# Kernel tuning notes

Measured on AMD Instinct MI355X. Metric: run time of the kernel, lower is better.

Reference implementation:

```python
import jax, jax.numpy as jnp
import numpy as np

N = 100000   # real nodes
E = 100000   # real edges (tree-like rumor cascades)
B = 128      # graphs in batch
IN = 256     # in_feats
HID = 128    # GCN hidden
OUT = 128    # out_feats


def setup_inputs() -> dict:
    key = jax.random.key(0)
    ks = jax.random.split(key, 16)
    sc = lambda k, sh: (jax.random.normal(k, sh, jnp.float32) * 0.05)
    x = jax.random.normal(ks[0], (N, IN), jnp.float32)
    edge_index = jax.random.randint(ks[1], (2, E), 0, N, jnp.int32)
    # sorted segment ids, every graph non-empty (equal split)
    batch = ((jnp.arange(N, dtype=jnp.int32) * B) // N).astype(jnp.int32)
    return {
        "x": x,
        "emb_w": sc(ks[2], (1, IN)),
        "td_w1": sc(ks[3], (IN, HID)), "td_b1": sc(ks[4], (HID,)),
        "td_w2": sc(ks[5], (HID, OUT)), "td_b2": sc(ks[6], (OUT,)),
        "bu_w1": sc(ks[7], (IN, HID)), "bu_b1": sc(ks[8], (HID,)),
        "bu_w2": sc(ks[9], (HID, OUT)), "bu_b2": sc(ks[10], (OUT,)),
        "p_w1": sc(ks[11], (2 * OUT, 256)), "p_b1": sc(ks[12], (256,)),
        "p_w2": sc(ks[13], (256, 128)), "p_b2": sc(ks[14], (128,)),
        "edge_index": edge_index,
        "batch": batch,
        "num_graphs": B,
    }


def gcn_conv(h, src, dst, W, b, n):
    # PyG GCNConv: transform, add self-loops, symmetric normalization, scatter-add
    h = h @ W
    loops = jnp.arange(n, dtype=src.dtype)
    s = jnp.concatenate([src, loops])
    d = jnp.concatenate([dst, loops])
    deg = jax.ops.segment_sum(jnp.ones(s.shape, h.dtype), d, num_segments=n)
    dinv = jax.lax.rsqrt(deg)  # deg >= 1 thanks to self-loops
    norm = dinv[s] * dinv[d]
    out = jax.ops.segment_sum(h[s] * norm[:, None], d, num_segments=n)
    return out + b


def reference(x, emb_w, td_w1, td_b1, td_w2, td_b2,
              bu_w1, bu_b1, bu_w2, bu_b2,
              p_w1, p_b1, p_w2, p_b2,
              edge_index, batch, num_graphs):
    n = x.shape[0]
    nv = n + 1  # with virtual node
    xv = jnp.concatenate([x, emb_w], axis=0)
    # root = first node of each graph (batch is sorted)
    roots = jnp.searchsorted(batch, jnp.arange(num_graphs, dtype=batch.dtype)).astype(edge_index.dtype)
    vsrc = jnp.full((num_graphs,), n, edge_index.dtype)
    src = jnp.concatenate([edge_index[0], vsrc])
    dst = jnp.concatenate([edge_index[1], roots])

    def branch(s, d, w1, b1, w2, b2):
        h = jax.nn.relu(gcn_conv(xv, s, d, w1, b1, nv))
        # dropout is identity in eval mode
        h = gcn_conv(h, s, d, w2, b2, nv)
        # Prompt=True: pool real nodes, add virtual-node embedding
        return jax.ops.segment_sum(h[:-1], batch, num_segments=num_graphs) + h[-1]

    td = branch(src, dst, td_w1, td_b1, td_w2, td_b2)
    bu = branch(dst, src, bu_w1, bu_b1, bu_w2, bu_b2)  # flipped edges
    h = jnp.concatenate([bu, td], axis=1)  # [B, 2*OUT]
    return jax.nn.relu(h @ p_w1 + p_b1) @ p_w2 + p_b2  # [B, 128]
```

## Files before the change

kernel.cpp:

```cpp
#include <hip/hip_runtime.h>

typedef __bf16 bf16_t;
typedef __bf16 bf16x8 __attribute__((ext_vector_type(8)));
typedef float f32x4 __attribute__((ext_vector_type(4)));

#define INF 256
#define HF 128
#define NPB 16
#define CHP 16
#define SLMASK 0x00FFFFFF
#define SCAN_STRIDE 512

__device__ inline float2 bf2_to_f2(unsigned v) {
    float lo = __uint_as_float(v << 16);
    float hi = __uint_as_float(v & 0xffff0000u);
    return make_float2(lo, hi);
}
__device__ inline unsigned f2_to_bf2(float a, float b) {
    __bf16 x = (__bf16)a, y = (__bf16)b;
    unsigned short ux = __builtin_bit_cast(unsigned short, x);
    unsigned short uy = __builtin_bit_cast(unsigned short, y);
    return (unsigned)ux | ((unsigned)uy << 16);
}

__global__ void k_init(const int* __restrict__ batch, int* __restrict__ roots,
                       int* __restrict__ Z, int N, int B, int zwords) {
    int i = blockIdx.x * blockDim.x + threadIdx.x;
    if (i < zwords) Z[i] = 0;
    if (i == 0) roots[B] = N;
    if (i < N) {
        if (i == 0) roots[batch[0]] = 0;
        else if (batch[i] != batch[i - 1]) roots[batch[i]] = i;
    }
}

__global__ void k_wswz2(const float* __restrict__ tw1, const float* __restrict__ bw1,
                        bf16_t* __restrict__ o) {
    int idx = blockIdx.x * blockDim.x + threadIdx.x;
    if (idx >= 65536) return;
    const float* W = (idx < 32768) ? tw1 : bw1;
    bf16_t* out = o + (idx & 32768);
    int i = idx & 32767;
    int j  = i & 7;
    int l  = (i >> 3) & 63;
    int t  = i >> 9;
    int n  = t & 7;
    int kk = t >> 3;
    int k  = kk * 32 + ((l >> 4) << 3) + j;
    int c  = (n << 4) + (l & 15);
    out[i] = (bf16_t)W[k * HF + c];
}

__global__ void k_degboth(const int* __restrict__ src, const int* __restrict__ dst,
                          const int* __restrict__ roots, int* __restrict__ indeg,
                          int E, int B, int N, int nv) {
    int e = blockIdx.x * blockDim.x + threadIdx.x;
    if (e >= E + B) return;
    int a, b;
    if (e < E) { a = src[e]; b = dst[e]; }
    else       { a = N;      b = roots[e - E]; }
    atomicAdd(&indeg[b], 1);
    atomicAdd(&indeg[nv + a], 1);
}

__global__ void k_dinvboth(const int* __restrict__ indeg, float* __restrict__ dinv, int n2) {
    int i = blockIdx.x * blockDim.x + threadIdx.x;
    if (i < n2) dinv[i] = rsqrtf(1.0f + (float)indeg[i]);
}

__global__ __launch_bounds__(256) void k_scan1(const int* __restrict__ indeg, int* __restrict__ bsum, int nv) {
    int dir = blockIdx.y;
    __shared__ int s[256];
    int t = threadIdx.x;
    int v = blockIdx.x * 256 + t;
    s[t] = (v < nv) ? indeg[dir * nv + v] : 0;
    __syncthreads();
    for (int off = 128; off > 0; off >>= 1) {
        if (t < off) s[t] += s[t + off];
        __syncthreads();
    }
    if (t == 0) bsum[dir * SCAN_STRIDE + blockIdx.x] = s[0];
}

__global__ __launch_bounds__(512) void k_scan2(int* __restrict__ bsum, int nblk) {
    int dir = blockIdx.y;
    int* p = bsum + dir * SCAN_STRIDE;
    __shared__ int s[512];
    int t = threadIdx.x;
    int v = (t < nblk) ? p[t] : 0;
    s[t] = v;
    __syncthreads();
    for (int off = 1; off < 512; off <<= 1) {
        int u = (t >= off) ? s[t - off] : 0;
        __syncthreads();
        s[t] += u;
        __syncthreads();
    }
    if (t < nblk) p[t] = s[t] - v;
}

__global__ __launch_bounds__(256) void k_scan3(const int* __restrict__ indeg, const int* __restrict__ bsum,
                                               int* __restrict__ off, int* __restrict__ cursor,
                                               int nv, int total) {
    int dir = blockIdx.y;
    __shared__ int s[256];
    int t = threadIdx.x;
    int v0 = blockIdx.x * 256 + t;
    int val = (v0 < nv) ? indeg[dir * nv + v0] : 0;
    s[t] = val;
    __syncthreads();
    for (int o = 1; o < 256; o <<= 1) {
        int u = (t >= o) ? s[t - o] : 0;
        __syncthreads();
        s[t] += u;
        __syncthreads();
    }
    int excl = s[t] - val + bsum[dir * SCAN_STRIDE + blockIdx.x];
    if (v0 < nv) {
        off[dir * (nv + 1) + v0] = excl;
        cursor[dir * nv + v0] = excl;
    }
    if (blockIdx.x == 0 && t == 0) off[dir * (nv + 1) + nv] = total;
}

__global__ void k_fill(const int* __restrict__ src, const int* __restrict__ dst,
                       const int* __restrict__ roots, int* __restrict__ cursor,
                       int* __restrict__ slots,
                       int E, int B, int N, int nv) {
    int e = blockIdx.x * blockDim.x + threadIdx.x;
    if (e >= E + B) return;
    int EB = E + B;
    int a, b;
    if (e < E) { a = src[e]; b = dst[e]; }
    else       { a = N;      b = roots[e - E]; }
    int p = atomicAdd(&cursor[b], 1);
    slots[p] = a | ((b & (NPB - 1)) << 24);
    p = atomicAdd(&cursor[nv + a], 1);
    slots[EB + p] = b | ((a & (NPB - 1)) << 24);
}

__global__ __launch_bounds__(512) void k_gemm1both(
    const float* __restrict__ x, const float* __restrict__ emb,
    const bf16_t* __restrict__ WfTD, const bf16_t* __restrict__ WfBU,
    const float* __restrict__ dinvTD, const float* __restrict__ dinvBU,
    bf16_t* __restrict__ rawsTD, bf16_t* __restrict__ rawsBU,
    int nv, int N)
{
    __shared__ bf16_t WS[8192];
    int lane = threadIdx.x & 63;
    int wave = threadIdx.x >> 6;
    int rowbase = blockIdx.x * 128 + wave * 16;
    int r = rowbase + (lane & 15);
    int kseg = lane >> 4;
    const float* xr = (r < N) ? (x + (size_t)r * INF) : emb;

    auto stage = [&](int kk) {
        #pragma unroll
        for (int q = 0; q < 2; ++q) {
            int idx = q * 512 + threadIdx.x;
            int d = idx >> 9, r9 = idx & 511;
            const bf16_t* Wsrc = d ? WfBU : WfTD;
            *reinterpret_cast<float4*>(WS + (size_t)idx * 8) =
                *reinterpret_cast<const float4*>(Wsrc + ((size_t)(kk << 9) + r9) * 8);
        }
    };

    bf16x8 a[8];
    #pragma unroll
    for (int h = 0; h < 2; ++h) {
        float4 f[8];
        #pragma unroll
        for (int kk = 0; kk < 4; ++kk) {
            int k0 = (h * 4 + kk) * 32 + kseg * 8;
            f[2 * kk]     = *reinterpret_cast<const float4*>(xr + k0);
            f[2 * kk + 1] = *reinterpret_cast<const float4*>(xr + k0 + 4);
        }
        #pragma unroll
        for (int kk = 0; kk < 4; ++kk) {
            bf16x8 av;
            av[0] = (__bf16)f[2 * kk].x;     av[1] = (__bf16)f[2 * kk].y;
            av[2] = (__bf16)f[2 * kk].z;     av[3] = (__bf16)f[2 * kk].w;
            av[4] = (__bf16)f[2 * kk + 1].x; av[5] = (__bf16)f[2 * kk + 1].y;
            av[6] = (__bf16)f[2 * kk + 1].z; av[7] = (__bf16)f[2 * kk + 1].w;
            a[h * 4 + kk] = av;
        }
    }

    f32x4 accT[8] = {}, accB[8] = {};
    #pragma unroll
    for (int kk = 0; kk < 8; ++kk) {
        stage(kk);
        __syncthreads();
        #pragma unroll
        for (int n = 0; n < 8; ++n) {
            bf16x8 bt = *reinterpret_cast<const bf16x8*>(WS + (size_t)(((n << 6) + lane)) * 8);
            accT[n] = __builtin_amdgcn_mfma_f32_16x16x32_bf16(a[kk], bt, accT[n], 0, 0, 0);
            bf16x8 bb = *reinterpret_cast<const bf16x8*>(WS + 4096 + (size_t)(((n << 6) + lane)) * 8);
            accB[n] = __builtin_amdgcn_mfma_f32_16x16x32_bf16(a[kk], bb, accB[n], 0, 0, 0);
        }
        if (kk < 7) __syncthreads();
    }

    int ccol = lane & 15;
    int cg = lane >> 4;
    #pragma unroll
    for (int i = 0; i < 4; ++i) {
        int rr = rowbase + cg * 4 + i;
        if (rr >= nv) continue;
        float diT = dinvTD[rr], diB = dinvBU[rr];
        bf16_t* oT = rawsTD + (size_t)rr * HF + ccol;
        bf16_t* oB = rawsBU + (size_t)rr * HF + ccol;
        #pragma unroll
        for (int n = 0; n < 8; ++n) {
            oT[n * 16] = (bf16_t)(accT[n][i] * diT);
            oB[n * 16] = (bf16_t)(accB[n][i] * diB);
        }
    }
}

__global__ __launch_bounds__(128) void k_gather1(
    const bf16_t* __restrict__ raws, const int* __restrict__ off,
    const int* __restrict__ slots,
    const float* __restrict__ dinv,
    const float* __restrict__ td_b1, const float* __restrict__ bu_b1,
    bf16_t* __restrict__ ab, int nv, int EB)
{
    int dir = blockIdx.y;
    const bf16_t* R  = raws + (size_t)dir * nv * HF;
    const int*    OF = off + (size_t)dir * (nv + 1);
    const int*    SL = slots + (size_t)dir * EB;
    const float*  DV = dinv + (size_t)dir * nv;
    const float*  bias = dir ? bu_b1 : td_b1;
    bf16_t* AB = ab + (size_t)dir * nv * HF;

    __shared__ float2 buf[2][NPB][64];
    int t = threadIdx.x;
    int h = t >> 6;
    int c = t & 63;
    int v0 = blockIdx.x * NPB;

    unsigned selfw[8];
    #pragma unroll
    for (int jj = 0; jj < 8; ++jj) {
        int v = min(v0 + 2 * jj + h, nv - 1);
        selfw[jj] = *reinterpret_cast<const unsigned*>(R + (size_t)v * HF + 2 * c);
    }
    __builtin_amdgcn_sched_barrier(0);
    #pragma unroll
    for (int jj = 0; jj < 8; ++jj) {
        float2 f = bf2_to_f2(selfw[jj]);
        buf[h][2 * jj + h][c] = f;
        buf[h][2 * jj + (1 - h)][c] = make_float2(0.f, 0.f);
    }

    int e0 = OF[v0], e1 = OF[min(v0 + NPB, nv)];
    #pragma unroll 1
    for (int i = e0; i < e1; i += 2 * CHP) {
        int w[CHP];
        #pragma unroll
        for (int u = 0; u < CHP; ++u) w[u] = SL[min(i + 2 * u + h, e1 - 1)];
        __builtin_amdgcn_sched_barrier(0);
        unsigned vw[CHP];
        #pragma unroll
        for (int u = 0; u < CHP; ++u)
            vw[u] = *reinterpret_cast<const unsigned*>(R + (size_t)(w[u] & SLMASK) * HF + 2 * c);
        __builtin_amdgcn_sched_barrier(0);
        #pragma unroll
        for (int u = 0; u < CHP; ++u) {
            if (i + 2 * u + h < e1) {
                float2 f = bf2_to_f2(vw[u]);
                int j = w[u] >> 24;
                float2 cur = buf[h][j][c];
                buf[h][j][c] = make_float2(cur.x + f.x, cur.y + f.y);
            }
        }
    }
    __syncthreads();

    float bs0 = bias[2 * c], bs1 = bias[2 * c + 1];
    #pragma unroll 1
    for (int jj = 0; jj < 8; ++jj) {
        int j = 2 * jj + h;
        int v = v0 + j;
        if (v >= nv) break;
        float2 a0 = buf[0][j][c], a1 = buf[1][j][c];
        float dv = DV[v];
        float x0 = dv * (a0.x + a1.x) + bs0;
        float x1 = dv * (a0.y + a1.y) + bs1;
        unsigned o = f2_to_bf2(dv * fmaxf(x0, 0.f), dv * fmaxf(x1, 0.f));
        *reinterpret_cast<unsigned*>(AB + (size_t)v * HF + 2 * c) = o;
    }
}

__global__ __launch_bounds__(128) void k_gather2pool(
    const bf16_t* __restrict__ ab, const int* __restrict__ off,
    const int* __restrict__ slots,
    const float* __restrict__ dinv, const int* __restrict__ batch,
    float* __restrict__ pooled, float* __restrict__ vrow,
    int nv, int EB, int N, int B)
{
    int dir = blockIdx.y;
    const bf16_t* S  = ab + (size_t)dir * nv * HF;
    const int*    OF = off + (size_t)dir * (nv + 1);
    const int*    SL = slots + (size_t)dir * EB;
    const float*  DV = dinv + (size_t)dir * nv;
    float* PP = pooled + (size_t)dir * B * HF;
    float* VR = vrow + dir * HF;

    __shared__ float2 buf[2][NPB][64];
    int t = threadIdx.x;
    int h = t >> 6;
    int c = t & 63;
    int v0 = blockIdx.x * NPB;

    unsigned selfw[8];
    #pragma unroll
    for (int jj = 0; jj < 8; ++jj) {
        int v = min(v0 + 2 * jj + h, nv - 1);
        selfw[jj] = *reinterpret_cast<const unsigned*>(S + (size_t)v * HF + 2 * c);
    }
    __builtin_amdgcn_sched_barrier(0);
    #pragma unroll
    for (int jj = 0; jj < 8; ++jj) {
        float2 f = bf2_to_f2(selfw[jj]);
        buf[h][2 * jj + h][c] = f;
        buf[h][2 * jj + (1 - h)][c] = make_float2(0.f, 0.f);
    }

    int e0 = OF[v0], e1 = OF[min(v0 + NPB, nv)];
    #pragma unroll 1
    for (int i = e0; i < e1; i += 2 * CHP) {
        int w[CHP];
        #pragma unroll
        for (int u = 0; u < CHP; ++u) w[u] = SL[min(i + 2 * u + h, e1 - 1)];
        __builtin_amdgcn_sched_barrier(0);
        unsigned vw[CHP];
        #pragma unroll
        for (int u = 0; u < CHP; ++u)
            vw[u] = *reinterpret_cast<const unsigned*>(S + (size_t)(w[u] & SLMASK) * HF + 2 * c);
        __builtin_amdgcn_sched_barrier(0);
        #pragma unroll
        for (int u = 0; u < CHP; ++u) {
            if (i + 2 * u + h < e1) {
                float2 f = bf2_to_f2(vw[u]);
                int j = w[u] >> 24;
                float2 cur = buf[h][j][c];
                buf[h][j][c] = make_float2(cur.x + f.x, cur.y + f.y);
            }
        }
    }
    __syncthreads();

    float acc0 = 0.f, acc1 = 0.f;
    int curg = -1;
    #pragma unroll 1
    for (int jj = 0; jj < 8; ++jj) {
        int j = 2 * jj + h;
        int v = v0 + j;
        if (v >= nv) break;
        float2 a0 = buf[0][j][c], a1 = buf[1][j][c];
        float dv = DV[v];
        float G0 = dv * (a0.x + a1.x);
        float G1 = dv * (a0.y + a1.y);
        if (v == N) { VR[2 * c] = G0; VR[2 * c + 1] = G1; continue; }
        int g = batch[v];
        if (g != curg) {
            if (curg >= 0) {
                atomicAdd(&PP[curg * HF + 2 * c], acc0);
                atomicAdd(&PP[curg * HF + 2 * c + 1], acc1);
            }
            curg = g; acc0 = 0.f; acc1 = 0.f;
        }
        acc0 += G0; acc1 += G1;
    }
    if (curg >= 0) {
        atomicAdd(&PP[curg * HF + 2 * c], acc0);
        atomicAdd(&PP[curg * HF + 2 * c + 1], acc1);
    }
}

__global__ __launch_bounds__(256) void k_mlp(
    const float* __restrict__ pooled, const float* __restrict__ vrow, const int* __restrict__ roots,
    const float* __restrict__ td_w2, const float* __restrict__ td_b2,
    const float* __restrict__ bu_w2, const float* __restrict__ bu_b2,
    const float* __restrict__ w1, const float* __restrict__ b1,
    const float* __restrict__ w2, const float* __restrict__ b2,
    float* __restrict__ out, int B)
{
    __shared__ float zsh[256];
    __shared__ float invec[256];
    __shared__ float hid[256];
    int g = blockIdx.x;
    int t = threadIdx.x;
    const float* pp_td = pooled;
    const float* pp_bu = pooled + (size_t)B * HF;
    const float* vr_td = vrow;
    const float* vr_bu = vrow + HF;
    zsh[t] = (t < 128) ? (pp_bu[g * HF + t] + vr_bu[t])
                       : (pp_td[g * HF + (t - 128)] + vr_td[t - 128]);
    __syncthreads();
    float cnt1 = (float)(roots[g + 1] - roots[g] + 1);
    float acc2;
    if (t < 128) {
        acc2 = cnt1 * bu_b2[t];
        #pragma unroll 8
        for (int k = 0; k < 128; ++k) acc2 = fmaf(zsh[k], bu_w2[k * HF + t], acc2);
    } else {
        int tt = t - 128;
        acc2 = cnt1 * td_b2[tt];
        #pragma unroll 8
        for (int k = 0; k < 128; ++k) acc2 = fmaf(zsh[128 + k], td_w2[k * HF + tt], acc2);
    }
    invec[t] = acc2;
    __syncthreads();
    float acc = b1[t];
    #pragma unroll 8
    for (int k = 0; k < 256; ++k) acc = fmaf(invec[k], w1[k * 256 + t], acc);
    hid[t] = acc > 0.f ? acc : 0.f;
    __syncthreads();
    if (t < 128) {
        float o = b2[t];
        #pragma unroll 8
        for (int k = 0; k < 256; ++k) o = fmaf(hid[k], w2[k * 128 + t], o);
        out[g * 128 + t] = o;
    }
}

extern "C" void kernel_launch(void* const* d_in, const int* in_sizes, int n_in,
                              void* d_out, int out_size, void* d_ws, size_t ws_size,
                              hipStream_t stream) {
    const float* x     = (const float*)d_in[0];
    const float* emb_w = (const float*)d_in[1];
    const float* td_w1 = (const float*)d_in[2];
    const float* td_b1 = (const float*)d_in[3];
    const float* td_w2 = (const float*)d_in[4];
    const float* td_b2 = (const float*)d_in[5];
    const float* bu_w1 = (const float*)d_in[6];
    const float* bu_b1 = (const float*)d_in[7];
    const float* bu_w2 = (const float*)d_in[8];
    const float* bu_b2 = (const float*)d_in[9];
    const float* p_w1  = (const float*)d_in[10];
    const float* p_b1  = (const float*)d_in[11];
    const float* p_w2  = (const float*)d_in[12];
    const float* p_b2  = (const float*)d_in[13];
    const int*   ei    = (const int*)d_in[14];
    const int*   batch = (const int*)d_in[15];

    int N = in_sizes[0] / INF;
    int E = in_sizes[14] / 2;
    int B = out_size / 128;
    int nv = N + 1;
    int EB = E + B;
    const int* src = ei;
    const int* dst = ei + E;

    char* wsp = (char*)d_ws;
    auto alloc = [&](size_t bytes) { char* p = wsp; wsp += (bytes + 255) & ~(size_t)255; return p; };
    int zwords = 2 * nv + 2 * B * HF + 2 * HF;
    int*    Z      = (int*)   alloc((size_t)zwords * 4);
    int*    indeg  = Z;
    float*  pooled = (float*)(Z + 2 * nv);
    float*  vrow   = pooled + 2 * B * HF;
    float*  dinv   = (float*) alloc((size_t)2 * nv * 4);
    int*    off    = (int*)   alloc((size_t)2 * (nv + 1) * 4);
    int*    cursor = (int*)   alloc((size_t)2 * nv * 4);
    int*    slots  = (int*)   alloc((size_t)2 * EB * 4);
    int*    bsum   = (int*)   alloc((size_t)2 * SCAN_STRIDE * 4);
    int*    roots  = (int*)   alloc((size_t)(B + 1) * 4);
    bf16_t* Wf     = (bf16_t*)alloc((size_t)65536 * 2);
    bf16_t* RAWS   = (bf16_t*)alloc((size_t)2 * nv * HF * 2);
    bf16_t* AB     = (bf16_t*)alloc((size_t)2 * nv * HF * 2);

    float* out = (float*)d_out;

    dim3 b256(256), b128(128);
    int nblk = (nv + 255) / 256;
    int ngb = (nv + NPB - 1) / NPB;
    int nvb = (nv + 127) / 128;
    int imax = max(zwords, N);

    k_init<<<dim3((imax + 255) / 256), b256, 0, stream>>>(batch, roots, Z, N, B, zwords);
    k_wswz2<<<dim3((65536 + 255) / 256), b256, 0, stream>>>(td_w1, bu_w1, Wf);
    k_degboth<<<dim3((EB + 255) / 256), b256, 0, stream>>>(src, dst, roots, indeg, E, B, N, nv);
    k_dinvboth<<<dim3((2 * nv + 255) / 256), b256, 0, stream>>>(indeg, dinv, 2 * nv);
    k_scan1<<<dim3(nblk, 2), b256, 0, stream>>>(indeg, bsum, nv);
    k_scan2<<<dim3(1, 2), dim3(512), 0, stream>>>(bsum, nblk);
    k_scan3<<<dim3(nblk, 2), b256, 0, stream>>>(indeg, bsum, off, cursor, nv, EB);
    k_fill<<<dim3((EB + 255) / 256), b256, 0, stream>>>(src, dst, roots, cursor, slots, E, B, N, nv);

    k_gemm1both<<<dim3(nvb), dim3(512), 0, stream>>>(
        x, emb_w, Wf, Wf + 32768, dinv, dinv + nv,
        RAWS, RAWS + (size_t)nv * HF, nv, N);

    k_gather1<<<dim3(ngb, 2), b128, 0, stream>>>(
        RAWS, off, slots, dinv, td_b1, bu_b1, AB, nv, EB);

    k_gather2pool<<<dim3(ngb, 2), b128, 0, stream>>>(
        AB, off, slots, dinv, batch, pooled, vrow, nv, EB, N, B);

    k_mlp<<<dim3(B), b256, 0, stream>>>(
        pooled, vrow, roots, td_w2, td_b2, bu_w2, bu_b2,
        p_w1, p_b1, p_w2, p_b2, out, B);
}
```

Baseline: 215.9 us.

## Make GEMM1 persistent with full weights resident in LDS and prefetched x rows

The first-layer GEMM kernel becomes persistent: 256 blocks each load both branch weight matrices (128 KB bf16) into LDS once, then loop over 128-row tiles with a stride of the grid size. Each iteration prefetches the next tile's x rows into registers while the MFMAs for the current tile run. This removes the per-k-step weight staging and the block barriers from the inner loop. In exchange, the 128 KB of LDS per block limits occupancy to one block per CU, register pressure rises from the prefetch buffer, and each block pays a large upfront weight load.

```diff
diff --git a/kernel.cpp b/kernel.cpp
--- a/kernel.cpp
+++ b/kernel.cpp
@@ -144,76 +144,94 @@
     const bf16_t* __restrict__ WfTD, const bf16_t* __restrict__ WfBU,
     const float* __restrict__ dinvTD, const float* __restrict__ dinvBU,
     bf16_t* __restrict__ rawsTD, bf16_t* __restrict__ rawsBU,
-    int nv, int N)
+    int nv, int N, int ntiles)
 {
-    __shared__ bf16_t WS[8192];
-    int lane = threadIdx.x & 63;
-    int wave = threadIdx.x >> 6;
-    int rowbase = blockIdx.x * 128 + wave * 16;
-    int r = rowbase + (lane & 15);
+    __shared__ bf16_t WS[65536];
+    int tid = threadIdx.x;
+    int lane = tid & 63;
+    int wave = tid >> 6;
     int kseg = lane >> 4;
-    const float* xr = (r < N) ? (x + (size_t)r * INF) : emb;
-
-    auto stage = [&](int kk) {
-        #pragma unroll
-        for (int q = 0; q < 2; ++q) {
-            int idx = q * 512 + threadIdx.x;
-            int d = idx >> 9, r9 = idx & 511;
-            const bf16_t* Wsrc = d ? WfBU : WfTD;
-            *reinterpret_cast<float4*>(WS + (size_t)idx * 8) =
-                *reinterpret_cast<const float4*>(Wsrc + ((size_t)(kk << 9) + r9) * 8);
-        }
-    };
-
-    bf16x8 a[8];
+    int rlane = lane & 15;
+
     #pragma unroll
-    for (int h = 0; h < 2; ++h) {
-        float4 f[8];
-        #pragma unroll
-        for (int kk = 0; kk < 4; ++kk) {
-            int k0 = (h * 4 + kk) * 32 + kseg * 8;
+    for (int q = 0; q < 32; ++q) {
+        int idx = q * 512 + tid;
+        int kk = idx >> 10;
+        int rem = idx & 1023;
+        int d = rem >> 9;
+        int nl = rem & 511;
+        const bf16_t* Wsrc = d ? WfBU : WfTD;
+        *reinterpret_cast<float4*>(WS + (size_t)idx * 8) =
+            *reinterpret_cast<const float4*>(Wsrc + (size_t)((kk << 9) + nl) * 8);
+    }
+    __syncthreads();
+
+    int tile = blockIdx.x;
+    if (tile >= ntiles) return;
+
+    float4 f[16];
+    {
+        int r = tile * 128 + wave * 16 + rlane;
+        const float* xr = (r < N) ? (x + (size_t)r * INF) : emb;
+        #pragma unroll
+        for (int kk = 0; kk < 8; ++kk) {
+            int k0 = kk * 32 + kseg * 8;
             f[2 * kk]     = *reinterpret_cast<const float4*>(xr + k0);
             f[2 * kk + 1] = *reinterpret_cast<const float4*>(xr + k0 + 4);
         }
-        #pragma unroll
-        for (int kk = 0; kk < 4; ++kk) {
+    }
+
+    #pragma unroll 1
+    for (; tile < ntiles; tile += gridDim.x) {
+        bf16x8 a[8];
+        #pragma unroll
+        for (int kk = 0; kk < 8; ++kk) {
             bf16x8 av;
             av[0] = (__bf16)f[2 * kk].x;     av[1] = (__bf16)f[2 * kk].y;
             av[2] = (__bf16)f[2 * kk].z;     av[3] = (__bf16)f[2 * kk].w;
             av[4] = (__bf16)f[2 * kk + 1].x; av[5] = (__bf16)f[2 * kk + 1].y;
             av[6] = (__bf16)f[2 * kk + 1].z; av[7] = (__bf16)f[2 * kk + 1].w;
-            a[h * 4 + kk] = av;
-        }
-    }
-
-    f32x4 accT[8] = {}, accB[8] = {};
-    #pragma unroll
-    for (int kk = 0; kk < 8; ++kk) {
-        stage(kk);
-        __syncthreads();
-        #pragma unroll
-        for (int n = 0; n < 8; ++n) {
-            bf16x8 bt = *reinterpret_cast<const bf16x8*>(WS + (size_t)(((n << 6) + lane)) * 8);
-            accT[n] = __builtin_amdgcn_mfma_f32_16x16x32_bf16(a[kk], bt, accT[n], 0, 0, 0);
-            bf16x8 bb = *reinterpret_cast<const bf16x8*>(WS + 4096 + (size_t)(((n << 6) + lane)) * 8);
-            accB[n] = __builtin_amdgcn_mfma_f32_16x16x32_bf16(a[kk], bb, accB[n], 0, 0, 0);
-        }
-        if (kk < 7) __syncthreads();
-    }
-
-    int ccol = lane & 15;
-    int cg = lane >> 4;
-    #pragma unroll
-    for (int i = 0; i < 4; ++i) {
-        int rr = rowbase + cg * 4 + i;
-        if (rr >= nv) continue;
-        float diT = dinvTD[rr], diB = dinvBU[rr];
-        bf16_t* oT = rawsTD + (size_t)rr * HF + ccol;
-        bf16_t* oB = rawsBU + (size_t)rr * HF + ccol;
-        #pragma unroll
-        for (int n = 0; n < 8; ++n) {
-            oT[n * 16] = (bf16_t)(accT[n][i] * diT);
-            oB[n * 16] = (bf16_t)(accB[n][i] * diB);
+            a[kk] = av;
+        }
+        int nt = tile + gridDim.x;
+        if (nt < ntiles) {
+            int r = nt * 128 + wave * 16 + rlane;
+            const float* xr = (r < N) ? (x + (size_t)r * INF) : emb;
+            #pragma unroll
+            for (int kk = 0; kk < 8; ++kk) {
+                int k0 = kk * 32 + kseg * 8;
+                f[2 * kk]     = *reinterpret_cast<const float4*>(xr + k0);
+                f[2 * kk + 1] = *reinterpret_cast<const float4*>(xr + k0 + 4);
+            }
+        }
+        f32x4 accT[8] = {}, accB[8] = {};
+        #pragma unroll
+        for (int kk = 0; kk < 8; ++kk) {
+            #pragma unroll
+            for (int n = 0; n < 8; ++n) {
+                bf16x8 bt = *reinterpret_cast<const bf16x8*>(
+                    WS + (size_t)((kk << 10) + (n << 6) + lane) * 8);
+                accT[n] = __builtin_amdgcn_mfma_f32_16x16x32_bf16(a[kk], bt, accT[n], 0, 0, 0);
+                bf16x8 bb = *reinterpret_cast<const bf16x8*>(
+                    WS + (size_t)((kk << 10) + 512 + (n << 6) + lane) * 8);
+                accB[n] = __builtin_amdgcn_mfma_f32_16x16x32_bf16(a[kk], bb, accB[n], 0, 0, 0);
+            }
+        }
+        int rowbase = tile * 128 + wave * 16;
+        int ccol = lane & 15;
+        int cg = lane >> 4;
+        #pragma unroll
+        for (int i = 0; i < 4; ++i) {
+            int rr = rowbase + cg * 4 + i;
+            if (rr >= nv) continue;
+            float diT = dinvTD[rr], diB = dinvBU[rr];
+            bf16_t* oT = rawsTD + (size_t)rr * HF + ccol;
+            bf16_t* oB = rawsBU + (size_t)rr * HF + ccol;
+            #pragma unroll
+            for (int n = 0; n < 8; ++n) {
+                oT[n * 16] = (bf16_t)(accT[n][i] * diT);
+                oB[n * 16] = (bf16_t)(accB[n][i] * diB);
+            }
         }
     }
 }
@@ -476,7 +494,7 @@
     dim3 b256(256), b128(128);
     int nblk = (nv + 255) / 256;
     int ngb = (nv + NPB - 1) / NPB;
-    int nvb = (nv + 127) / 128;
+    int ntiles = (nv + 127) / 128;
     int imax = max(zwords, N);
 
     k_init<<<dim3((imax + 255) / 256), b256, 0, stream>>>(batch, roots, Z, N, B, zwords);
@@ -488,9 +506,9 @@
     k_scan3<<<dim3(nblk, 2), b256, 0, stream>>>(indeg, bsum, off, cursor, nv, EB);
     k_fill<<<dim3((EB + 255) / 256), b256, 0, stream>>>(src, dst, roots, cursor, slots, E, B, N, nv);
 
-    k_gemm1both<<<dim3(nvb), dim3(512), 0, stream>>>(
+    k_gemm1both<<<dim3(256), dim3(512), 0, stream>>>(
         x, emb_w, Wf, Wf + 32768, dinv, dinv + nv,
-        RAWS, RAWS + (size_t)nv * HF, nv, N);
+        RAWS, RAWS + (size_t)nv * HF, nv, N, ntiles);
 
     k_gather1<<<dim3(ngb, 2), b128, 0, stream>>>(
         RAWS, off, slots, dinv, td_b1, bu_b1, AB, nv, EB);
```

After: 438.7 us. 103% more time.

## Double-buffer GEMM weight staging and prefetch edge slot indices in aggregation

Applied to the files above, without the earlier changes.

The first-layer GEMM now stages weights into two shared-memory buffers, so the next k-slice is loaded while MFMAs run on the current one. This removes one barrier per iteration and doubles LDS use for the weights. Both sparse aggregation kernels now load the next chunk of neighbour slot indices before processing the current gathered rows, to overlap the dependent index-then-row load latency. This costs extra registers for the prefetched indices.

```diff
diff --git a/kernel.cpp b/kernel.cpp
--- a/kernel.cpp
+++ b/kernel.cpp
@@ -146,7 +146,7 @@
     bf16_t* __restrict__ rawsTD, bf16_t* __restrict__ rawsBU,
     int nv, int N)
 {
-    __shared__ bf16_t WS[8192];
+    __shared__ bf16_t WS[2 * 8192];
     int lane = threadIdx.x & 63;
     int wave = threadIdx.x >> 6;
     int rowbase = blockIdx.x * 128 + wave * 16;
@@ -154,13 +154,13 @@
     int kseg = lane >> 4;
     const float* xr = (r < N) ? (x + (size_t)r * INF) : emb;
 
-    auto stage = [&](int kk) {
+    auto stage = [&](int kk, int buf) {
         #pragma unroll
         for (int q = 0; q < 2; ++q) {
             int idx = q * 512 + threadIdx.x;
             int d = idx >> 9, r9 = idx & 511;
             const bf16_t* Wsrc = d ? WfBU : WfTD;
-            *reinterpret_cast<float4*>(WS + (size_t)idx * 8) =
+            *reinterpret_cast<float4*>(WS + (size_t)(buf * 8192 + idx * 8)) =
                 *reinterpret_cast<const float4*>(Wsrc + ((size_t)(kk << 9) + r9) * 8);
         }
     };
@@ -186,16 +186,20 @@
         }
     }
 
+    stage(0, 0);
+    __syncthreads();
+
     f32x4 accT[8] = {}, accB[8] = {};
     #pragma unroll
     for (int kk = 0; kk < 8; ++kk) {
-        stage(kk);
-        __syncthreads();
+        int cur = kk & 1;
+        if (kk < 7) stage(kk + 1, cur ^ 1);
+        const bf16_t* wb = WS + cur * 8192;
         #pragma unroll
         for (int n = 0; n < 8; ++n) {
-            bf16x8 bt = *reinterpret_cast<const bf16x8*>(WS + (size_t)(((n << 6) + lane)) * 8);
+            bf16x8 bt = *reinterpret_cast<const bf16x8*>(wb + (size_t)(((n << 6) + lane)) * 8);
             accT[n] = __builtin_amdgcn_mfma_f32_16x16x32_bf16(a[kk], bt, accT[n], 0, 0, 0);
-            bf16x8 bb = *reinterpret_cast<const bf16x8*>(WS + 4096 + (size_t)(((n << 6) + lane)) * 8);
+            bf16x8 bb = *reinterpret_cast<const bf16x8*>(wb + 4096 + (size_t)(((n << 6) + lane)) * 8);
             accB[n] = __builtin_amdgcn_mfma_f32_16x16x32_bf16(a[kk], bb, accB[n], 0, 0, 0);
         }
         if (kk < 7) __syncthreads();
@@ -254,16 +258,24 @@
     }
 
     int e0 = OF[v0], e1 = OF[min(v0 + NPB, nv)];
+    int w[CHP];
+    if (e0 < e1) {
+        #pragma unroll
+        for (int u = 0; u < CHP; ++u) w[u] = SL[min(e0 + 2 * u + h, e1 - 1)];
+    }
     #pragma unroll 1
     for (int i = e0; i < e1; i += 2 * CHP) {
-        int w[CHP];
-        #pragma unroll
-        for (int u = 0; u < CHP; ++u) w[u] = SL[min(i + 2 * u + h, e1 - 1)];
         __builtin_amdgcn_sched_barrier(0);
         unsigned vw[CHP];
         #pragma unroll
         for (int u = 0; u < CHP; ++u)
             vw[u] = *reinterpret_cast<const unsigned*>(R + (size_t)(w[u] & SLMASK) * HF + 2 * c);
+        int wn[CHP];
+        int inx = i + 2 * CHP;
+        if (inx < e1) {
+            #pragma unroll
+            for (int u = 0; u < CHP; ++u) wn[u] = SL[min(inx + 2 * u + h, e1 - 1)];
+        }
         __builtin_amdgcn_sched_barrier(0);
         #pragma unroll
         for (int u = 0; u < CHP; ++u) {
@@ -274,6 +286,8 @@
                 buf[h][j][c] = make_float2(cur.x + f.x, cur.y + f.y);
             }
         }
+        #pragma unroll
+        for (int u = 0; u < CHP; ++u) w[u] = wn[u];
     }
     __syncthreads();
 
@@ -328,16 +342,24 @@
     }
 
     int e0 = OF[v0], e1 = OF[min(v0 + NPB, nv)];
+    int w[CHP];
+    if (e0 < e1) {
+        #pragma unroll
+        for (int u = 0; u < CHP; ++u) w[u] = SL[min(e0 + 2 * u + h, e1 - 1)];
+    }
     #pragma unroll 1
     for (int i = e0; i < e1; i += 2 * CHP) {
-        int w[CHP];
-        #pragma unroll
-        for (int u = 0; u < CHP; ++u) w[u] = SL[min(i + 2 * u + h, e1 - 1)];
         __builtin_amdgcn_sched_barrier(0);
         unsigned vw[CHP];
         #pragma unroll
         for (int u = 0; u < CHP; ++u)
             vw[u] = *reinterpret_cast<const unsigned*>(S + (size_t)(w[u] & SLMASK) * HF + 2 * c);
+        int wn[CHP];
+        int inx = i + 2 * CHP;
+        if (inx < e1) {
+            #pragma unroll
+            for (int u = 0; u < CHP; ++u) wn[u] = SL[min(inx + 2 * u + h, e1 - 1)];
+        }
         __builtin_amdgcn_sched_barrier(0);
         #pragma unroll
         for (int u = 0; u < CHP; ++u) {
@@ -348,6 +370,8 @@
                 buf[h][j][c] = make_float2(cur.x + f.x, cur.y + f.y);
             }
         }
+        #pragma unroll
+        for (int u = 0; u < CHP; ++u) w[u] = wn[u];
     }
     __syncthreads();
 
```

Measured after the change: 214.2 us. Within noise of the previous version (-0.8%).
